# Performance work log

Hardware: AMD Instinct MI355X
Metric: run time of the kernel (lower is better)

## Reference

```python
import jax, jax.numpy as jnp
import numpy as np

C = 32        # channels after first 1x1 conv
HEADS = 4     # FuncSelfAttention heads ('channel' head split -> d = C // HEADS)


def setup_inputs() -> dict:
    key = jax.random.key(0)
    ks = jax.random.split(key, 8)
    B, H, W = 8, 512, 512
    s = 0.1
    return {
        "x": jax.random.normal(ks[0], (B, 1, H, W), jnp.float32),
        "n": 8,
        "m": 8,
        # Conv2d(1, C, kernel_size=1) == per-pixel linear 1->C
        "w1": jax.random.normal(ks[1], (C, 1), jnp.float32) * s,
        "b1": jax.random.normal(ks[2], (C,), jnp.float32) * s,
        # fused QKV projection over channels, bias=False
        "wqkv": jax.random.normal(ks[3], (3 * C, C), jnp.float32) * s,
        # output projection of the attention
        "wproj": jax.random.normal(ks[4], (C, C), jnp.float32) * s,
        "bproj": jax.random.normal(ks[5], (C,), jnp.float32) * s,
        # Conv2d(C, 1, kernel_size=1)
        "w2": jax.random.normal(ks[6], (1, C), jnp.float32) * s,
        "b2": jax.random.normal(ks[7], (1,), jnp.float32) * s,
    }


def reference(x, n, m, w1, b1, wqkv, wproj, bproj, w2, b2):
    B, _, H, W = x.shape
    d = C // HEADS
    hh, ww = H // n, W // m
    S, P = n * m, hh * ww  # subdomain tokens, quadrature points per token

    # 1x1 conv (pointwise linear over channel dim)
    h = jnp.einsum('oi,bihw->bohw', w1, x) + b1[None, :, None, None]

    # decompose2d: [B,C,H,W] -> [B, n*m, C, hh, ww] (flatten spatial per token)
    u = h.reshape(B, C, n, hh, m, ww).transpose(0, 2, 4, 1, 3, 5)
    u = u.reshape(B, S, C, P)

    # channel self-attention over subdomain functions
    qkv = jnp.einsum('oc,bscp->bsop', wqkv, u)          # [B,S,3C,P]
    q, k, v = jnp.split(qkv, 3, axis=2)
    q = q.reshape(B, S, HEADS, d, P)
    k = k.reshape(B, S, HEADS, d, P)
    v = v.reshape(B, S, HEADS, d, P)

    # L2 (quadrature-mean) inner product over points + head channels
    scale = 1.0 / (P * np.sqrt(d).astype(np.float32))
    scores = jnp.einsum('bihdp,bjhdp->bhij', q, k) * scale  # [B,H,S,S]
    attn = jax.nn.softmax(scores, axis=-1)
    o = jnp.einsum('bhij,bjhdp->bihdp', attn, v).reshape(B, S, C, P)
    o = jnp.einsum('oc,bscp->bsop', wproj, o) + bproj[None, None, :, None]

    # recompose2d: [B, n*m, C, hh, ww] -> [B, C, H, W]
    o = o.reshape(B, n, m, C, hh, ww).transpose(0, 3, 1, 4, 2, 5)
    o = o.reshape(B, C, H, W)

    # final 1x1 conv C -> 1
    out = jnp.einsum('oc,bchw->bohw', w2, o) + b2[None, :, None, None]
    return out
```

## Files before the change

### kernel.cpp

```cpp
#include <hip/hip_runtime.h>


#define CONST_OFF 0
#define SXP_OFF   16
#define WB_OFF    (16 + 128*64)
#define PART_OFF  (WB_OFF + 8*2048)

typedef __attribute__((ext_vector_type(8))) short bf16x8;
typedef __attribute__((ext_vector_type(4))) float f32x4;

__device__ __forceinline__ unsigned short f2bf(float f) {
    unsigned int u = __float_as_uint(f);
    u = (u + 0x7FFFu + ((u >> 16) & 1u)) >> 16;
    return (unsigned short)u;
}

__global__ __launch_bounds__(256) void k1_gram(const float* __restrict__ x,
                                               float* __restrict__ ws)
{
    __shared__ unsigned short xsb[64 * 272];
    int b = blockIdx.x >> 4, prg = blockIdx.x & 15;
    int t = threadIdx.x;
    const float* xb = x + (size_t)b * 262144;

    #pragma unroll
    for (int prl = 0; prl < 4; ++prl) {
        int pr = prg * 4 + prl;
        #pragma unroll
        for (int k = 0; k < 4; ++k) {
            int q = t + 256 * k;
            int tj = q >> 7, col4 = q & 127;
            float4 v = *(const float4*)(xb + (tj * 64 + pr) * 512 + col4 * 4);
            int token = tj * 8 + (col4 >> 4);
            ushort4 h;
            h.x = f2bf(v.x); h.y = f2bf(v.y); h.z = f2bf(v.z); h.w = f2bf(v.w);
            *(ushort4*)(&xsb[token * 272 + prl * 64 + (col4 & 15) * 4]) = h;
        }
    }
    __syncthreads();

    if (t < 64) {
        const uint4* p = (const uint4*)(&xsb[t * 272]);
        float s = 0.f;
        #pragma unroll
        for (int c = 0; c < 32; ++c) {
            uint4 u = p[c];
            s += __uint_as_float(u.x << 16) + __uint_as_float(u.x & 0xFFFF0000u)
               + __uint_as_float(u.y << 16) + __uint_as_float(u.y & 0xFFFF0000u)
               + __uint_as_float(u.z << 16) + __uint_as_float(u.z & 0xFFFF0000u)
               + __uint_as_float(u.w << 16) + __uint_as_float(u.w & 0xFFFF0000u);
        }
        ws[SXP_OFF + blockIdx.x * 64 + t] = s;
    }

    int w = t >> 6, lane = t & 63;
    int m = lane & 15, quad = lane >> 4;
    f32x4 acc[4];
    #pragma unroll
    for (int jq = 0; jq < 4; ++jq) acc[jq] = (f32x4){0.f, 0.f, 0.f, 0.f};

    #pragma unroll
    for (int s = 0; s < 8; ++s) {
        int kb = s * 32 + quad * 8;
        bf16x8 a = *(const bf16x8*)(&xsb[(w * 16 + m) * 272 + kb]);
        #pragma unroll
        for (int jq = 0; jq < 4; ++jq) {
            bf16x8 bb = *(const bf16x8*)(&xsb[(jq * 16 + m) * 272 + kb]);
            acc[jq] = __builtin_amdgcn_mfma_f32_16x16x32_bf16(a, bb, acc[jq],
                                                              0, 0, 0);
        }
    }

    float* part = ws + PART_OFF + (size_t)blockIdx.x * 4096;
    #pragma unroll
    for (int jq = 0; jq < 4; ++jq)
        #pragma unroll
        for (int r = 0; r < 4; ++r)
            part[(w * 16 + quad * 4 + r) * 64 + jq * 16 + m] = acc[jq][r];
}

__global__ __launch_bounds__(256) void k2_attn(
    const float* __restrict__ w1, const float* __restrict__ b1,
    const float* __restrict__ wqkv, const float* __restrict__ wproj,
    const float* __restrict__ bproj, const float* __restrict__ w2,
    const float* __restrict__ b2, float* __restrict__ ws)
{
    __shared__ float arow[96], crow[96], pvec[32];
    __shared__ float cst[16];
    __shared__ float G_s[8 * 65];
    __shared__ float sxp_s[4][64];
    __shared__ float sx_s[64];
    __shared__ float coef_s[4][8];
    __shared__ float m_s[4][8];
    int b = blockIdx.x >> 3, rg = blockIdx.x & 7;
    int t = threadIdx.x;

    if (t < 96) {
        float sa = 0.f, sc = 0.f;
        for (int c = 0; c < 32; ++c) {
            float w = wqkv[t * 32 + c];
            sa += w * w1[c];
            sc += w * b1[c];
        }
        arow[t] = sa; crow[t] = sc;
    } else if (t < 128) {
        int c = t - 96;
        float s = 0.f;
        for (int oc = 0; oc < 32; ++oc) s += w2[oc] * wproj[oc * 32 + c];
        pvec[c] = s;
    }

    {
        const float* p0 = ws + PART_OFF + (size_t)(b * 16) * 4096 + rg * 512;
        float a0 = 0.f, a1 = 0.f;
        #pragma unroll
        for (int r = 0; r < 16; ++r) {
            const float* pr = p0 + (size_t)r * 4096;
            a0 += pr[t]; a1 += pr[t + 256];
        }
        int e0 = t;          G_s[(e0 >> 6) * 65 + (e0 & 63)] = a0;
        int e1 = t + 256;    G_s[(e1 >> 6) * 65 + (e1 & 63)] = a1;
    }

    {
        int j = t & 63, r4 = t >> 6;
        float s = 0.f;
        #pragma unroll
        for (int k = 0; k < 4; ++k)
            s += ws[SXP_OFF + (b * 16 + r4 * 4 + k) * 64 + j];
        sxp_s[r4][j] = s;
    }
    __syncthreads();
    if (t < 64)
        sx_s[t] = sxp_s[0][t] + sxp_s[1][t] + sxp_s[2][t] + sxp_s[3][t];

    const float scale = 1.0f / (4096.0f * 2.8284271247461903f);
    if (t >= 64 && t < 68) {
        int h = t - 64;
        float A = 0.f, Bk = 0.f, g = 0.f;
        #pragma unroll
        for (int dd = 0; dd < 8; ++dd) {
            int o = h * 8 + dd;
            A  += arow[o] * arow[32 + o];
            Bk += crow[o] * arow[32 + o];
            g  += pvec[o] * arow[64 + o];
        }
        cst[h]     = A * scale;
        cst[4 + h] = Bk * scale;
        cst[8 + h] = g;
    } else if (t == 68) {
        float c0 = b2[0];
        for (int c = 0; c < 32; ++c)  c0 += pvec[c] * crow[64 + c];
        for (int oc = 0; oc < 32; ++oc) c0 += w2[oc] * bproj[oc];
        cst[12] = c0;
    }
    __syncthreads();

    if (t < 32) {
        int h = t >> 3, il = t & 7;
        float A  = cst[h];
        float Bk = cst[4 + h];
        float g  = cst[8 + h];
        float m = -1e30f;
        for (int j = 0; j < 64; ++j) {
            float s = A * G_s[il * 65 + j] + Bk * sx_s[j];
            m = fmaxf(m, s);
        }
        float Z = 0.f;
        for (int j = 0; j < 64; ++j) {
            float s = A * G_s[il * 65 + j] + Bk * sx_s[j];
            Z += __expf(s - m);
        }
        coef_s[h][il] = g / Z;
        m_s[h][il]    = m;
    }
    __syncthreads();

    {
        float A0 = cst[0], A1 = cst[1], A2 = cst[2], A3 = cst[3];
        float B0 = cst[4], B1 = cst[5], B2 = cst[6], B3 = cst[7];
        unsigned short* wout =
            (unsigned short*)(ws + WB_OFF) + b * 4096 + rg * 512;
        #pragma unroll
        for (int k = 0; k < 2; ++k) {
            int e = t + 256 * k;
            int il = e >> 6, j = e & 63;
            float G  = G_s[il * 65 + j];
            float sx = sx_s[j];
            float w =
                coef_s[0][il] * __expf(A0 * G + B0 * sx - m_s[0][il]) +
                coef_s[1][il] * __expf(A1 * G + B1 * sx - m_s[1][il]) +
                coef_s[2][il] * __expf(A2 * G + B2 * sx - m_s[2][il]) +
                coef_s[3][il] * __expf(A3 * G + B3 * sx - m_s[3][il]);
            wout[e] = f2bf(w);
        }
    }
    if (b == 0 && rg == 0 && t == 68) ws[CONST_OFF + 12] = cst[12];
}

__global__ __launch_bounds__(256) void k3_apply(const float* __restrict__ x,
                                                const float* __restrict__ ws,
                                                float* __restrict__ out)
{
    __shared__ unsigned short xt[64 * 72];
    __shared__ unsigned short wsm[64 * 72];
    int b = blockIdx.x >> 6, pr = blockIdx.x & 63;
    int t = threadIdx.x;
    const float* xb = x + (size_t)b * 262144;

    #pragma unroll
    for (int k = 0; k < 4; ++k) {
        int q = t + 256 * k;
        int j = q >> 4, c4 = q & 15;
        int ti = j >> 3, tk = j & 7;
        float4 v = *(const float4*)(xb + (ti * 64 + pr) * 512 + tk * 64 + c4 * 4);
        xt[(4 * c4 + 0) * 72 + j] = f2bf(v.x);
        xt[(4 * c4 + 1) * 72 + j] = f2bf(v.y);
        xt[(4 * c4 + 2) * 72 + j] = f2bf(v.z);
        xt[(4 * c4 + 3) * 72 + j] = f2bf(v.w);
    }
    {
        const uint4* wb = (const uint4*)((const unsigned short*)(ws + WB_OFF)
                                         + b * 4096);
        #pragma unroll
        for (int k = 0; k < 2; ++k) {
            int q = t + 256 * k;
            int i = q >> 3, j8 = q & 7;
            *(uint4*)(&wsm[i * 72 + j8 * 8]) = wb[q];
        }
    }
    __syncthreads();

    int w = t >> 6, lane = t & 63;
    int m = lane & 15, quad = lane >> 4;
    f32x4 acc[4];
    #pragma unroll
    for (int jq = 0; jq < 4; ++jq) acc[jq] = (f32x4){0.f, 0.f, 0.f, 0.f};

    #pragma unroll
    for (int s = 0; s < 2; ++s) {
        int kb = s * 32 + quad * 8;
        bf16x8 a = *(const bf16x8*)(&wsm[(w * 16 + m) * 72 + kb]);
        #pragma unroll
        for (int jq = 0; jq < 4; ++jq) {
            bf16x8 bv = *(const bf16x8*)(&xt[(jq * 16 + m) * 72 + kb]);
            acc[jq] = __builtin_amdgcn_mfma_f32_16x16x32_bf16(a, bv, acc[jq],
                                                              0, 0, 0);
        }
    }

    float c0 = ws[CONST_OFF + 12];
    float* ob = out + (size_t)b * 262144;
    #pragma unroll
    for (int jq = 0; jq < 4; ++jq)
        #pragma unroll
        for (int r = 0; r < 4; ++r) {
            int i = w * 16 + quad * 4 + r;
            int c = jq * 16 + m;
            int ti = i >> 3, tk = i & 7;
            ob[(ti * 64 + pr) * 512 + tk * 64 + c] = acc[jq][r] + c0;
        }
}

extern "C" void kernel_launch(void* const* d_in, const int* in_sizes, int n_in,
                              void* d_out, int out_size, void* d_ws, size_t ws_size,
                              hipStream_t stream) {
    const float* x     = (const float*)d_in[0];
    const float* w1    = (const float*)d_in[3];
    const float* b1    = (const float*)d_in[4];
    const float* wqkv  = (const float*)d_in[5];
    const float* wproj = (const float*)d_in[6];
    const float* bproj = (const float*)d_in[7];
    const float* w2    = (const float*)d_in[8];
    const float* b2    = (const float*)d_in[9];
    float* out = (float*)d_out;
    float* ws  = (float*)d_ws;

    k1_gram<<<128, 256, 0, stream>>>(x, ws);
    k2_attn<<<64, 256, 0, stream>>>(w1, b1, wqkv, wproj, bproj, w2, b2, ws);
    k3_apply<<<512, 256, 0, stream>>>(x, ws, out);
}
```

Before: 88.23 us.

## Split gram over more blocks, parallelize softmax stats, swizzle apply LDS

The gram kernel now uses 256 blocks, each covering 2 pixel rows instead of 4, with every global load issued before conversion, and k2 reduces over twice as many partials. The softmax max and sum in k2 now use all 256 threads with shuffle reductions in place of 32 serial threads. k3 prefetches the weight tile into registers, batches its x loads, and XOR-swizzles the transposed LDS tile to cut bank conflicts. The added partials mean more workspace traffic and a longer reduction in k2.

```diff
diff --git a/kernel.cpp b/kernel.cpp
--- a/kernel.cpp
+++ b/kernel.cpp
@@ -3,7 +3,7 @@
 
 #define CONST_OFF 0
 #define SXP_OFF   16
-#define WB_OFF    (16 + 128*64)
+#define WB_OFF    (16 + 256*64)
 #define PART_OFF  (WB_OFF + 8*2048)
 
 typedef __attribute__((ext_vector_type(8))) short bf16x8;
@@ -18,32 +18,36 @@
 __global__ __launch_bounds__(256) void k1_gram(const float* __restrict__ x,
                                                float* __restrict__ ws)
 {
-    __shared__ unsigned short xsb[64 * 272];
-    int b = blockIdx.x >> 4, prg = blockIdx.x & 15;
+    __shared__ unsigned short xsb[64 * 136];
+    int b = blockIdx.x >> 5, prg2 = blockIdx.x & 31;
     int t = threadIdx.x;
     const float* xb = x + (size_t)b * 262144;
 
-    #pragma unroll
-    for (int prl = 0; prl < 4; ++prl) {
-        int pr = prg * 4 + prl;
-        #pragma unroll
-        for (int k = 0; k < 4; ++k) {
-            int q = t + 256 * k;
-            int tj = q >> 7, col4 = q & 127;
-            float4 v = *(const float4*)(xb + (tj * 64 + pr) * 512 + col4 * 4);
-            int token = tj * 8 + (col4 >> 4);
-            ushort4 h;
-            h.x = f2bf(v.x); h.y = f2bf(v.y); h.z = f2bf(v.z); h.w = f2bf(v.w);
-            *(ushort4*)(&xsb[token * 272 + prl * 64 + (col4 & 15) * 4]) = h;
-        }
+    float4 v[8];
+    #pragma unroll
+    for (int u = 0; u < 8; ++u) {
+        int q = t + 256 * u;
+        int prl = q >> 10, rem = q & 1023;
+        int tj = rem >> 7, col4 = rem & 127;
+        v[u] = *(const float4*)(xb + (tj * 64 + prg2 * 2 + prl) * 512 + col4 * 4);
+    }
+    #pragma unroll
+    for (int u = 0; u < 8; ++u) {
+        int q = t + 256 * u;
+        int prl = q >> 10, rem = q & 1023;
+        int tj = rem >> 7, col4 = rem & 127;
+        int token = tj * 8 + (col4 >> 4);
+        ushort4 h;
+        h.x = f2bf(v[u].x); h.y = f2bf(v[u].y); h.z = f2bf(v[u].z); h.w = f2bf(v[u].w);
+        *(ushort4*)(&xsb[token * 136 + prl * 64 + (col4 & 15) * 4]) = h;
     }
     __syncthreads();
 
     if (t < 64) {
-        const uint4* p = (const uint4*)(&xsb[t * 272]);
+        const uint4* p = (const uint4*)(&xsb[t * 136]);
         float s = 0.f;
         #pragma unroll
-        for (int c = 0; c < 32; ++c) {
+        for (int c = 0; c < 16; ++c) {
             uint4 u = p[c];
             s += __uint_as_float(u.x << 16) + __uint_as_float(u.x & 0xFFFF0000u)
                + __uint_as_float(u.y << 16) + __uint_as_float(u.y & 0xFFFF0000u)
@@ -60,12 +64,12 @@
     for (int jq = 0; jq < 4; ++jq) acc[jq] = (f32x4){0.f, 0.f, 0.f, 0.f};
 
     #pragma unroll
-    for (int s = 0; s < 8; ++s) {
+    for (int s = 0; s < 4; ++s) {
         int kb = s * 32 + quad * 8;
-        bf16x8 a = *(const bf16x8*)(&xsb[(w * 16 + m) * 272 + kb]);
+        bf16x8 a = *(const bf16x8*)(&xsb[(w * 16 + m) * 136 + kb]);
         #pragma unroll
         for (int jq = 0; jq < 4; ++jq) {
-            bf16x8 bb = *(const bf16x8*)(&xsb[(jq * 16 + m) * 272 + kb]);
+            bf16x8 bb = *(const bf16x8*)(&xsb[(jq * 16 + m) * 136 + kb]);
             acc[jq] = __builtin_amdgcn_mfma_f32_16x16x32_bf16(a, bb, acc[jq],
                                                               0, 0, 0);
         }
@@ -111,10 +115,10 @@
     }
 
     {
-        const float* p0 = ws + PART_OFF + (size_t)(b * 16) * 4096 + rg * 512;
+        const float* p0 = ws + PART_OFF + (size_t)(b * 32) * 4096 + rg * 512;
         float a0 = 0.f, a1 = 0.f;
         #pragma unroll
-        for (int r = 0; r < 16; ++r) {
+        for (int r = 0; r < 32; ++r) {
             const float* pr = p0 + (size_t)r * 4096;
             a0 += pr[t]; a1 += pr[t + 256];
         }
@@ -126,8 +130,8 @@
         int j = t & 63, r4 = t >> 6;
         float s = 0.f;
         #pragma unroll
-        for (int k = 0; k < 4; ++k)
-            s += ws[SXP_OFF + (b * 16 + r4 * 4 + k) * 64 + j];
+        for (int k = 0; k < 8; ++k)
+            s += ws[SXP_OFF + (b * 32 + r4 * 8 + k) * 64 + j];
         sxp_s[r4][j] = s;
     }
     __syncthreads();
@@ -156,23 +160,33 @@
     }
     __syncthreads();
 
-    if (t < 32) {
-        int h = t >> 3, il = t & 7;
+    {
+        int pair = t >> 3, jg = t & 7;
+        int h = pair >> 3, il = pair & 7;
         float A  = cst[h];
         float Bk = cst[4 + h];
-        float g  = cst[8 + h];
-        float m = -1e30f;
-        for (int j = 0; j < 64; ++j) {
+        float sv[8];
+        float mloc = -1e30f;
+        #pragma unroll
+        for (int jj = 0; jj < 8; ++jj) {
+            int j = jg * 8 + jj;
             float s = A * G_s[il * 65 + j] + Bk * sx_s[j];
-            m = fmaxf(m, s);
-        }
-        float Z = 0.f;
-        for (int j = 0; j < 64; ++j) {
-            float s = A * G_s[il * 65 + j] + Bk * sx_s[j];
-            Z += __expf(s - m);
-        }
-        coef_s[h][il] = g / Z;
-        m_s[h][il]    = m;
+            sv[jj] = s;
+            mloc = fmaxf(mloc, s);
+        }
+        mloc = fmaxf(mloc, __shfl_xor(mloc, 1));
+        mloc = fmaxf(mloc, __shfl_xor(mloc, 2));
+        mloc = fmaxf(mloc, __shfl_xor(mloc, 4));
+        float z = 0.f;
+        #pragma unroll
+        for (int jj = 0; jj < 8; ++jj) z += __expf(sv[jj] - mloc);
+        z += __shfl_xor(z, 1);
+        z += __shfl_xor(z, 2);
+        z += __shfl_xor(z, 4);
+        if (jg == 0) {
+            coef_s[h][il] = cst[8 + h] / z;
+            m_s[h][il]    = mloc;
+        }
     }
     __syncthreads();
 
@@ -208,25 +222,37 @@
     int t = threadIdx.x;
     const float* xb = x + (size_t)b * 262144;
 
+    const uint4* wb = (const uint4*)((const unsigned short*)(ws + WB_OFF)
+                                     + b * 4096);
+    uint4 wv[2];
+    #pragma unroll
+    for (int k = 0; k < 2; ++k) wv[k] = wb[t + 256 * k];
+
+    float4 v[4];
     #pragma unroll
     for (int k = 0; k < 4; ++k) {
         int q = t + 256 * k;
         int j = q >> 4, c4 = q & 15;
         int ti = j >> 3, tk = j & 7;
-        float4 v = *(const float4*)(xb + (ti * 64 + pr) * 512 + tk * 64 + c4 * 4);
-        xt[(4 * c4 + 0) * 72 + j] = f2bf(v.x);
-        xt[(4 * c4 + 1) * 72 + j] = f2bf(v.y);
-        xt[(4 * c4 + 2) * 72 + j] = f2bf(v.z);
-        xt[(4 * c4 + 3) * 72 + j] = f2bf(v.w);
-    }
-    {
-        const uint4* wb = (const uint4*)((const unsigned short*)(ws + WB_OFF)
-                                         + b * 4096);
+        v[k] = *(const float4*)(xb + (ti * 64 + pr) * 512 + tk * 64 + c4 * 4);
+    }
+
+    #pragma unroll
+    for (int k = 0; k < 4; ++k) {
+        int q = t + 256 * k;
+        int j = q >> 4, c4 = q & 15;
+        int jx = j ^ ((c4 & 7) << 3);
+        xt[(4 * c4 + 0) * 72 + jx] = f2bf(v[k].x);
+        xt[(4 * c4 + 1) * 72 + jx] = f2bf(v[k].y);
+        xt[(4 * c4 + 2) * 72 + jx] = f2bf(v[k].z);
+        xt[(4 * c4 + 3) * 72 + jx] = f2bf(v[k].w);
+    }
+    {
         #pragma unroll
         for (int k = 0; k < 2; ++k) {
             int q = t + 256 * k;
             int i = q >> 3, j8 = q & 7;
-            *(uint4*)(&wsm[i * 72 + j8 * 8]) = wb[q];
+            *(uint4*)(&wsm[i * 72 + j8 * 8]) = wv[k];
         }
     }
     __syncthreads();
@@ -243,7 +269,9 @@
         bf16x8 a = *(const bf16x8*)(&wsm[(w * 16 + m) * 72 + kb]);
         #pragma unroll
         for (int jq = 0; jq < 4; ++jq) {
-            bf16x8 bv = *(const bf16x8*)(&xt[(jq * 16 + m) * 72 + kb]);
+            int row = jq * 16 + m;
+            int kbx = kb ^ (((row >> 2) & 7) << 3);
+            bf16x8 bv = *(const bf16x8*)(&xt[row * 72 + kbx]);
             acc[jq] = __builtin_amdgcn_mfma_f32_16x16x32_bf16(a, bv, acc[jq],
                                                               0, 0, 0);
         }
@@ -276,7 +304,7 @@
     float* out = (float*)d_out;
     float* ws  = (float*)d_ws;
 
-    k1_gram<<<128, 256, 0, stream>>>(x, ws);
+    k1_gram<<<256, 256, 0, stream>>>(x, ws);
     k2_attn<<<64, 256, 0, stream>>>(w1, b1, wqkv, wproj, bproj, w2, b2, ws);
     k3_apply<<<512, 256, 0, stream>>>(x, ws, out);
 }
```

After: 88.79 us. About the same (+0.6%).
